# Kernel tuning notes

Hardware: AMD Instinct MI355X
Metric: run time of the kernel (lower is better)

## Reference

```python
import jax, jax.numpy as jnp
import numpy as np

V, D, H, B, LK, LQ, PAD = 10000, 300, 512, 16, 64, 64, 0


def _lstm(x, Wih, Whh, b, h0, c0):
    # x: [B,T,D]; Wih: [4G,D]; Whh: [4G,G]; b: [4G] (b_ih+b_hh); torch gate order i,f,g,o
    xg = jnp.einsum('btd,gd->btg', x, Wih) + b
    def step(hc, xt):
        h, c = hc
        g = xt + h @ Whh.T
        i, f, gg, o = jnp.split(g, 4, axis=-1)
        c = jax.nn.sigmoid(f) * c + jax.nn.sigmoid(i) * jnp.tanh(gg)
        h = jax.nn.sigmoid(o) * jnp.tanh(c)
        return (h, c), h
    (hT, cT), hs = jax.lax.scan(step, (h0, c0), jnp.swapaxes(xg, 0, 1))
    return jnp.swapaxes(hs, 0, 1), hT, cT


def setup_inputs() -> dict:
    key = jax.random.key(0)
    ks = jax.random.split(key, 24)
    n = lambda k, s: (jax.random.normal(k, s, jnp.float32) * 0.05)
    return {
        'source': jax.random.randint(ks[0], (B, LK), 0, V),
        'prev_outputs': jax.random.randint(ks[1], (B, LQ), 0, V),
        'emb': n(ks[2], (V, D)),
        'enc_f_Wih': n(ks[3], (4 * H, D)), 'enc_f_Whh': n(ks[4], (4 * H, H)), 'enc_f_b': n(ks[5], (4 * H,)),
        'enc_b_Wih': n(ks[6], (4 * H, D)), 'enc_b_Whh': n(ks[7], (4 * H, H)), 'enc_b_b': n(ks[8], (4 * H,)),
        'dec_Wih': n(ks[9], (8 * H, D)), 'dec_Whh': n(ks[10], (8 * H, 2 * H)), 'dec_b': n(ks[11], (8 * H,)),
        'k_W': n(ks[12], (2 * H, 2 * H)), 'k_b': n(ks[13], (2 * H,)),
        'v_W': n(ks[14], (2 * H, 2 * H)), 'v_b': n(ks[15], (2 * H,)),
        'fc1_W': n(ks[16], (2 * H, 4 * H)), 'fc1_b': n(ks[17], (2 * H,)),
        'fc2_W': n(ks[18], (V, 2 * H)), 'fc2_b': n(ks[19], (V,)),
    }


def reference(source, prev_outputs, emb, enc_f_Wih, enc_f_Whh, enc_f_b,
              enc_b_Wih, enc_b_Whh, enc_b_b, dec_Wih, dec_Whh, dec_b,
              k_W, k_b, v_W, v_b, fc1_W, fc1_b, fc2_W, fc2_b):
    bsz = source.shape[0]
    xs = emb[source]  # [B,LK,300]
    z = jnp.zeros((bsz, H), xs.dtype)
    out_f, hf, cf = _lstm(xs, enc_f_Wih, enc_f_Whh, enc_f_b, z, z)
    out_b, hb, cb = _lstm(xs[:, ::-1], enc_b_Wih, enc_b_Whh, enc_b_b, z, z)
    enc_out = jnp.concatenate([out_f, out_b[:, ::-1]], axis=-1)  # [B,LK,1024]
    # self.change: interleave fwd/bwd channels -> [B,1024]
    h0 = jnp.stack([hf, hb], axis=-1).reshape(bsz, 2 * H)
    c0 = jnp.stack([cf, cb], axis=-1).reshape(bsz, 2 * H)
    Q, _, _ = _lstm(emb[prev_outputs], dec_Wih, dec_Whh, dec_b, h0, c0)  # [B,LQ,1024]
    K = enc_out @ k_W.T + k_b
    Vv = enc_out @ v_W.T + v_b
    M = jnp.einsum('bqc,bkc->bqk', Q, K)
    mask = (source == PAD)[:, None, :]
    M = jnp.where(mask, -jnp.inf, M)
    A = jax.nn.softmax(M, axis=2)
    ctx = jnp.einsum('bqk,bkc->bqc', A, Vv)  # == (A[...,None]*V[:,None]).sum(2)
    x = jnp.tanh(jnp.concatenate([ctx, Q], axis=-1) @ fc1_W.T + fc1_b)  # dropout=identity (eval)
    return x @ fc2_W.T + fc2_b
```

## Files before the change

### kernel.cpp

```cpp
#include <hip/hip_runtime.h>
#include <cmath>

#define BB   16
#define LKK  64
#define LQQ  64
#define DD   300
#define HH   512
#define H2   1024
#define G4   2048
#define G8   4096
#define VV   10000

__device__ __forceinline__ float sigmoidf_(float x) { return 1.f / (1.f + expf(-x)); }

typedef __attribute__((ext_vector_type(4))) float    f4_;
typedef __attribute__((ext_vector_type(4))) unsigned u4_;

__device__ __forceinline__ void st_sc(float* p, float v) {
    __hip_atomic_store(p, v, __ATOMIC_RELAXED, __HIP_MEMORY_SCOPE_AGENT);
}

__device__ __forceinline__ f4_ ld4_sc(const float* p) {
    f4_ r;
    asm volatile("global_load_dwordx4 %0, %1, off sc0 sc1" : "=v"(r) : "v"(p));
    return r;
}
__device__ __forceinline__ u4_ ld4u_sc(const unsigned* p) {
    u4_ r;
    asm volatile("global_load_dwordx4 %0, %1, off sc0 sc1" : "=v"(r) : "v"(p));
    return r;
}
__device__ __forceinline__ void wait_vm0() {
    asm volatile("s_waitcnt vmcnt(0)" ::: "memory");
    __builtin_amdgcn_sched_barrier(0);
}

__device__ __forceinline__ void gbar2(unsigned* flags, int wg, unsigned target) {
    asm volatile("s_waitcnt vmcnt(0)" ::: "memory");
    if (threadIdx.x == 0)
        __hip_atomic_store(&flags[wg], target, __ATOMIC_RELAXED, __HIP_MEMORY_SCOPE_AGENT);
    if (threadIdx.x < 64) {
        for (;;) {
            u4_ f = ld4u_sc(flags + (threadIdx.x << 2));
            wait_vm0();
            unsigned m0 = f[0] < f[1] ? f[0] : f[1];
            unsigned m1 = f[2] < f[3] ? f[2] : f[3];
            unsigned mn = m0 < m1 ? m0 : m1;
            if (__all((int)(mn >= target))) break;
            __builtin_amdgcn_s_sleep(1);
        }
    }
    __syncthreads();
}

__global__ void rev_idx_kernel(const int* __restrict__ src, int* __restrict__ rev,
                               unsigned* __restrict__ bars) {
    int tid = blockIdx.x * blockDim.x + threadIdx.x;
    if (tid < 512) bars[tid] = 0u;
    if (tid < BB * LKK) {
        int b = tid / LKK, t = tid % LKK;
        rev[tid] = src[b * LKK + (LKK - 1 - t)];
    }
}

typedef __attribute__((ext_vector_type(8))) short bfrag8;
typedef __attribute__((ext_vector_type(4))) float facc4;

__device__ __forceinline__ unsigned short f2bf(float x) {
    unsigned u = __float_as_uint(x);
    unsigned r = (u + 0x7fffu + ((u >> 16) & 1u)) >> 16;
    return (unsigned short)r;
}

#define ASTR 40

__device__ __forceinline__ void gemm_core(
        short* __restrict__ Ah, short* __restrict__ Al,
        short* __restrict__ Bh, short* __restrict__ Bl,
        const float* __restrict__ A, const int* __restrict__ gidx, int lda,
        const float* __restrict__ Bw, int ldb,
        const float* __restrict__ bias,
        float* __restrict__ C, int ldc,
        int N, int K, int act, int m0, int n0) {
    int tid = threadIdx.x;
    int lane = tid & 63, w = tid >> 6;
    int wr = w >> 1, wc = w & 1;
    int fr = lane & 15, fg = lane >> 4;

    int sr = tid >> 1, sc = (tid & 1) << 4;
    long abase = gidx ? (long)gidx[m0 + sr] * lda : (long)(m0 + sr) * lda;
    int gn = n0 + sr;
    bool bval = gn < N;
    long bbase = (long)gn * ldb;

    facc4 acc[4][4] = {};

    for (int k0 = 0; k0 < K; k0 += 32) {
        {
            float v[16];
            if (k0 + sc + 16 <= K) {
                const float* ap = A + abase + k0 + sc;
                float4 t0 = *(const float4*)(ap + 0);
                float4 t1 = *(const float4*)(ap + 4);
                float4 t2 = *(const float4*)(ap + 8);
                float4 t3 = *(const float4*)(ap + 12);
                v[0]=t0.x; v[1]=t0.y; v[2]=t0.z;  v[3]=t0.w;
                v[4]=t1.x; v[5]=t1.y; v[6]=t1.z;  v[7]=t1.w;
                v[8]=t2.x; v[9]=t2.y; v[10]=t2.z; v[11]=t2.w;
                v[12]=t3.x; v[13]=t3.y; v[14]=t3.z; v[15]=t3.w;
            } else {
#pragma unroll
                for (int c = 0; c < 16; c++) {
                    int k = k0 + sc + c;
                    v[c] = (k < K) ? A[abase + k] : 0.f;
                }
            }
            bfrag8 h0, h1, l0, l1;
#pragma unroll
            for (int c = 0; c < 8; c++) {
                unsigned short hb = f2bf(v[c]);
                float hf = __uint_as_float(((unsigned)hb) << 16);
                h0[c] = (short)hb; l0[c] = (short)f2bf(v[c] - hf);
            }
#pragma unroll
            for (int c = 0; c < 8; c++) {
                unsigned short hb = f2bf(v[8 + c]);
                float hf = __uint_as_float(((unsigned)hb) << 16);
                h1[c] = (short)hb; l1[c] = (short)f2bf(v[8 + c] - hf);
            }
            *(bfrag8*)&Ah[sr * ASTR + sc]     = h0;
            *(bfrag8*)&Ah[sr * ASTR + sc + 8] = h1;
            *(bfrag8*)&Al[sr * ASTR + sc]     = l0;
            *(bfrag8*)&Al[sr * ASTR + sc + 8] = l1;
        }
        {
            float v[16];
            if (bval && (k0 + sc + 16 <= K)) {
                const float* bp = Bw + bbase + k0 + sc;
                float4 t0 = *(const float4*)(bp + 0);
                float4 t1 = *(const float4*)(bp + 4);
                float4 t2 = *(const float4*)(bp + 8);
                float4 t3 = *(const float4*)(bp + 12);
                v[0]=t0.x; v[1]=t0.y; v[2]=t0.z;  v[3]=t0.w;
                v[4]=t1.x; v[5]=t1.y; v[6]=t1.z;  v[7]=t1.w;
                v[8]=t2.x; v[9]=t2.y; v[10]=t2.z; v[11]=t2.w;
                v[12]=t3.x; v[13]=t3.y; v[14]=t3.z; v[15]=t3.w;
            } else {
#pragma unroll
                for (int c = 0; c < 16; c++) {
                    int k = k0 + sc + c;
                    v[c] = (bval && k < K) ? Bw[bbase + k] : 0.f;
                }
            }
            bfrag8 h0, h1, l0, l1;
#pragma unroll
            for (int c = 0; c < 8; c++) {
                unsigned short hb = f2bf(v[c]);
                float hf = __uint_as_float(((unsigned)hb) << 16);
                h0[c] = (short)hb; l0[c] = (short)f2bf(v[c] - hf);
            }
#pragma unroll
            for (int c = 0; c < 8; c++) {
                unsigned short hb = f2bf(v[8 + c]);
                float hf = __uint_as_float(((unsigned)hb) << 16);
                h1[c] = (short)hb; l1[c] = (short)f2bf(v[8 + c] - hf);
            }
            *(bfrag8*)&Bh[sr * ASTR + sc]     = h0;
            *(bfrag8*)&Bh[sr * ASTR + sc + 8] = h1;
            *(bfrag8*)&Bl[sr * ASTR + sc]     = l0;
            *(bfrag8*)&Bl[sr * ASTR + sc + 8] = l1;
        }
        __syncthreads();

        bfrag8 ah[4], al[4], bh[4], bl[4];
#pragma unroll
        for (int i = 0; i < 4; i++) {
            int ar = wr * 64 + i * 16 + fr;
            ah[i] = *(const bfrag8*)&Ah[ar * ASTR + fg * 8];
            al[i] = *(const bfrag8*)&Al[ar * ASTR + fg * 8];
            int br = wc * 64 + i * 16 + fr;
            bh[i] = *(const bfrag8*)&Bh[br * ASTR + fg * 8];
            bl[i] = *(const bfrag8*)&Bl[br * ASTR + fg * 8];
        }
#pragma unroll
        for (int i = 0; i < 4; i++)
#pragma unroll
            for (int j = 0; j < 4; j++) {
                acc[i][j] = __builtin_amdgcn_mfma_f32_16x16x32_bf16(ah[i], bh[j], acc[i][j], 0, 0, 0);
                acc[i][j] = __builtin_amdgcn_mfma_f32_16x16x32_bf16(ah[i], bl[j], acc[i][j], 0, 0, 0);
                acc[i][j] = __builtin_amdgcn_mfma_f32_16x16x32_bf16(al[i], bh[j], acc[i][j], 0, 0, 0);
            }
        __syncthreads();
    }

#pragma unroll
    for (int i = 0; i < 4; i++) {
        int row = m0 + wr * 64 + i * 16 + fg * 4;
#pragma unroll
        for (int j = 0; j < 4; j++) {
            int col = n0 + wc * 64 + j * 16 + fr;
            if (col < N) {
                float bz = bias[col];
#pragma unroll
                for (int q = 0; q < 4; q++) {
                    float vv = acc[i][j][q] + bz;
                    if (act == 1) vv = tanhf(vv);
                    C[(long)(row + q) * ldc + col] = vv;
                }
            }
        }
    }
}

__global__ __launch_bounds__(256)
void gemm_mfma128(const float* __restrict__ A, const int* __restrict__ gidx, int lda,
                  const float* __restrict__ Bw, int ldb,
                  const float* __restrict__ bias,
                  float* __restrict__ C, int ldc,
                  int N, int K, int act) {
    __shared__ __align__(16) short Ah[128 * ASTR];
    __shared__ __align__(16) short Al[128 * ASTR];
    __shared__ __align__(16) short Bh[128 * ASTR];
    __shared__ __align__(16) short Bl[128 * ASTR];
    gemm_core(Ah, Al, Bh, Bl, A, gidx, lda, Bw, ldb, bias, C, ldc, N, K, act,
              blockIdx.x * 128, blockIdx.y * 128);
}

__global__ __launch_bounds__(256)
void gemm_kv(const float* __restrict__ enc_out,
             const float* __restrict__ kW, const float* __restrict__ kb,
             const float* __restrict__ vW, const float* __restrict__ vb,
             float* __restrict__ Kbuf, float* __restrict__ Vbuf) {
    __shared__ __align__(16) short Ah[128 * ASTR];
    __shared__ __align__(16) short Al[128 * ASTR];
    __shared__ __align__(16) short Bh[128 * ASTR];
    __shared__ __align__(16) short Bl[128 * ASTR];
    int ny = blockIdx.y;
    if (ny < 8)
        gemm_core(Ah, Al, Bh, Bl, enc_out, nullptr, H2, kW, H2, kb, Kbuf, H2,
                  H2, H2, 0, blockIdx.x * 128, ny * 128);
    else
        gemm_core(Ah, Al, Bh, Bl, enc_out, nullptr, H2, vW, H2, vb, Vbuf, H2,
                  H2, H2, 0, blockIdx.x * 128, (ny - 8) * 128);
}

__global__ __launch_bounds__(256)
void gemm_xg(const float* __restrict__ emb,
             const int* __restrict__ src, const int* __restrict__ rev,
             const int* __restrict__ prev,
             const float* __restrict__ Wf, const float* __restrict__ bf,
             const float* __restrict__ Wb, const float* __restrict__ bb,
             const float* __restrict__ Wd, const float* __restrict__ bd,
             float* __restrict__ xf, float* __restrict__ xb,
             float* __restrict__ xd) {
    __shared__ __align__(16) short Ah[128 * ASTR];
    __shared__ __align__(16) short Al[128 * ASTR];
    __shared__ __align__(16) short Bh[128 * ASTR];
    __shared__ __align__(16) short Bl[128 * ASTR];
    int ny = blockIdx.y;
    if (ny < 16)
        gemm_core(Ah, Al, Bh, Bl, emb, src, DD, Wf, DD, bf, xf, G4,
                  G4, DD, 0, blockIdx.x * 128, ny * 128);
    else if (ny < 32)
        gemm_core(Ah, Al, Bh, Bl, emb, rev, DD, Wb, DD, bb, xb, G4,
                  G4, DD, 0, blockIdx.x * 128, (ny - 16) * 128);
    else
        gemm_core(Ah, Al, Bh, Bl, emb, prev, DD, Wd, DD, bd, xd, G8,
                  G8, DD, 0, blockIdx.x * 128, (ny - 32) * 128);
}

__global__ __launch_bounds__(256, 1)
void enc_recur(const float* __restrict__ xg_f, const float* __restrict__ xg_b,
               const float* __restrict__ Wf, const float* __restrict__ Wb,
               float* __restrict__ hglob, float* __restrict__ enc_out,
               float* __restrict__ encc, unsigned* __restrict__ flags) {
    __shared__ float hs[HH * 16];
    __shared__ float red[256 * 33];
    __shared__ float g256[256];
    __shared__ float hout[64];
    int wg  = blockIdx.x;
    int dir = wg >> 7;
    int j0  = (wg & 127) * 4;
    int tid = threadIdx.x;
    int ks   = tid & 31;
    int tile = tid >> 5;
    int bh   = tile >> 2;
    int gate = tile & 3;
    int sw   = (ks >> 2) & 3;
    const float* W  = dir ? Wb : Wf;
    const float* xg = dir ? xg_b : xg_f;

    float wreg[4][16];
#pragma unroll
    for (int jn = 0; jn < 4; jn++) {
        const float* wrow = W + (long)(gate * HH + j0 + jn) * HH;
#pragma unroll
        for (int j = 0; j < 16; j++) wreg[jn][j] = wrow[ks + 32 * j];
    }

    int ub = tid & 15, ujj = tid >> 4;
    int xb = tid >> 4, xgate = (tid >> 2) & 3, xjn = tid & 3;
    float creg = 0.f;
    float4* hsv = (float4*)hs;

    for (int t = 0; t < LKK; t++) {
        float acc[8][4];
#pragma unroll
        for (int i = 0; i < 8; i++)
#pragma unroll
            for (int jn = 0; jn < 4; jn++) acc[i][jn] = 0.f;

        auto do_fma = [&](int jlo, int jhi) {
#pragma unroll
            for (int j = jlo; j < jhi; j++) {
                int k = ks + 32 * j;
                float4 h0 = hsv[k * 4 + ((bh * 2 + 0) ^ sw)];
                float4 h1 = hsv[k * 4 + ((bh * 2 + 1) ^ sw)];
#pragma unroll
                for (int jn = 0; jn < 4; jn++) {
                    float w = wreg[jn][j];
                    acc[0][jn] += h0.x * w; acc[1][jn] += h0.y * w;
                    acc[2][jn] += h0.z * w; acc[3][jn] += h0.w * w;
                    acc[4][jn] += h1.x * w; acc[5][jn] += h1.y * w;
                    acc[6][jn] += h1.z * w; acc[7][jn] += h1.w * w;
                }
            }
        };

        float xval = xg[(long)(xb * LKK + t) * G4 + xgate * HH + j0 + xjn];

        if (t == 0) {
            for (int i = tid; i < HH * 16; i += 256) hs[i] = 0.f;
            __syncthreads();
            do_fma(0, 16);
        } else {
            const float* hg = hglob + (long)((dir << 1) | (t & 1)) * (HH * 16);
            f4_ vv[8];
#pragma unroll
            for (int u = 0; u < 8; u++) vv[u] = ld4_sc(hg + tid * 4 + u * 1024);
            asm volatile("s_waitcnt vmcnt(4)" ::: "memory");
            __builtin_amdgcn_sched_barrier(0);
#pragma unroll
            for (int u = 0; u < 4; u++) {
                int e = tid * 4 + u * 1024;
                int jj = e >> 4, b0 = e & 15;
                *(f4_*)&hs[(jj << 4) + ((((b0 >> 2) ^ ((jj >> 2) & 3))) << 2)] = vv[u];
            }
            __syncthreads();
            do_fma(0, 8);
            wait_vm0();
#pragma unroll
            for (int u = 4; u < 8; u++) {
                int e = tid * 4 + u * 1024;
                int jj = e >> 4, b0 = e & 15;
                *(f4_*)&hs[(jj << 4) + ((((b0 >> 2) ^ ((jj >> 2) & 3))) << 2)] = vv[u];
            }
            __syncthreads();
            do_fma(8, 16);
        }

#pragma unroll
        for (int i = 0; i < 8; i++)
#pragma unroll
            for (int jn = 0; jn < 4; jn++)
                red[((bh * 8 + i) * 16 + gate * 4 + jn) * 33 + ks] = acc[i][jn];
        __syncthreads();
        {
            const float* row = red + tid * 33;
            float s0 = 0.f, s1 = 0.f, s2 = 0.f, s3 = 0.f;
#pragma unroll
            for (int u = 0; u < 8; u++) {
                s0 += row[u * 4 + 0]; s1 += row[u * 4 + 1];
                s2 += row[u * 4 + 2]; s3 += row[u * 4 + 3];
            }
            g256[tid] = ((s0 + s1) + (s2 + s3)) + xval;
        }
        __syncthreads();

        if (tid < 64) {
            int j = j0 + ujj;
            float gi = g256[ub * 16 + 0  + ujj];
            float gf = g256[ub * 16 + 4  + ujj];
            float gg = g256[ub * 16 + 8  + ujj];
            float go = g256[ub * 16 + 12 + ujj];
            float cv = sigmoidf_(gf) * creg + sigmoidf_(gi) * tanhf(gg);
            creg = cv;
            float hv = sigmoidf_(go) * tanhf(cv);
            st_sc(&hglob[(long)((dir << 1) | ((t + 1) & 1)) * (HH * 16) + j * 16 + ub], hv);
            hout[tid] = hv;
            if (t == LKK - 1) encc[(dir * BB + ub) * HH + j] = creg;
        }
        if (t < LKK - 1) gbar2(flags, wg, (unsigned)(t + 1));
        else __syncthreads();
        if (tid >= 64 && tid < 128) {
            int lt = tid - 64;
            int j = j0 + (lt >> 4);
            int kpos = dir ? (LKK - 1 - t) : t;
            enc_out[(long)((lt & 15) * LKK + kpos) * H2 + dir * HH + j] = hout[lt];
        }
    }
}

__global__ __launch_bounds__(256, 1)
void dec_recur(const float* __restrict__ xg_d, const float* __restrict__ Wd,
               const float* __restrict__ enc_out, const float* __restrict__ encc,
               float* __restrict__ hglob, float* __restrict__ Qout,
               unsigned* __restrict__ flags) {
    __shared__ float hs[HH * 16];
    __shared__ float red[256 * 33];
    __shared__ float g256[256];
    __shared__ float hout[64];
    int wg  = blockIdx.x;
    int j0  = wg * 4;
    int tid = threadIdx.x;
    int ks   = tid & 31;
    int tile = tid >> 5;
    int bh   = tile >> 2;
    int gate = tile & 3;
    int sw   = (ks >> 2) & 3;

    float wreg[4][32];
#pragma unroll
    for (int jn = 0; jn < 4; jn++) {
        const float* wrow = Wd + (long)(gate * H2 + j0 + jn) * H2;
#pragma unroll
        for (int j = 0; j < 32; j++) wreg[jn][j] = wrow[ks + 32 * j];
    }

    int ub = tid & 15, ujj = tid >> 4;
    int xb = tid >> 4, xgate = (tid >> 2) & 3, xjn = tid & 3;
    float creg = 0.f;
    if (tid < 64) {
        int j = j0 + ujj;
        creg = ((j & 1) == 0) ? encc[ub * HH + (j >> 1)]
                              : encc[(BB + ub) * HH + (j >> 1)];
    }
    float4* hsv = (float4*)hs;

    for (int t = 0; t < LQQ; t++) {
        float xval = xg_d[(long)(xb * LQQ + t) * G8 + xgate * H2 + j0 + xjn];
        float acc[8][4];
#pragma unroll
        for (int i = 0; i < 8; i++)
#pragma unroll
            for (int jn = 0; jn < 4; jn++) acc[i][jn] = 0.f;

        auto do_fma = [&](int half) {
#pragma unroll
            for (int jj2 = 0; jj2 < 16; jj2++) {
                int j = half * 16 + jj2;
                int kl = ks + 32 * jj2;
                float4 h0 = hsv[kl * 4 + ((bh * 2 + 0) ^ sw)];
                float4 h1 = hsv[kl * 4 + ((bh * 2 + 1) ^ sw)];
#pragma unroll
                for (int jn = 0; jn < 4; jn++) {
                    float w = wreg[jn][j];
                    acc[0][jn] += h0.x * w; acc[1][jn] += h0.y * w;
                    acc[2][jn] += h0.z * w; acc[3][jn] += h0.w * w;
                    acc[4][jn] += h1.x * w; acc[5][jn] += h1.y * w;
                    acc[6][jn] += h1.z * w; acc[7][jn] += h1.w * w;
                }
            }
        };

        if (t == 0) {
            for (int half = 0; half < 2; half++) {
                for (int e = tid; e < HH * 16; e += 256) {
                    int kl = e >> 4, b = e & 15;
                    int k = half * HH + kl;
                    float hv = ((k & 1) == 0)
                        ? enc_out[(long)(b * LKK + (LKK - 1)) * H2 + (k >> 1)]
                        : enc_out[(long)(b * LKK) * H2 + HH + (k >> 1)];
                    hs[(kl << 4) + ((((b >> 2) ^ ((kl >> 2) & 3))) << 2) + (b & 3)] = hv;
                }
                __syncthreads();
                do_fma(half);
                __syncthreads();
            }
        } else {
            const float* hgA = hglob + (long)(t & 1) * (H2 * 16);
            f4_ vvA[8], vvB[8];
#pragma unroll
            for (int u = 0; u < 8; u++) vvA[u] = ld4_sc(hgA + tid * 4 + u * 1024);
#pragma unroll
            for (int u = 0; u < 8; u++) vvB[u] = ld4_sc(hgA + (HH * 16) + tid * 4 + u * 1024);
            asm volatile("s_waitcnt vmcnt(8)" ::: "memory");
            __builtin_amdgcn_sched_barrier(0);
#pragma unroll
            for (int u = 0; u < 8; u++) {
                int e = tid * 4 + u * 1024;
                int kl = e >> 4, b0 = e & 15;
                *(f4_*)&hs[(kl << 4) + ((((b0 >> 2) ^ ((kl >> 2) & 3))) << 2)] = vvA[u];
            }
            __syncthreads();
            do_fma(0);
            __syncthreads();
            wait_vm0();
#pragma unroll
            for (int u = 0; u < 8; u++) {
                int e = tid * 4 + u * 1024;
                int kl = e >> 4, b0 = e & 15;
                *(f4_*)&hs[(kl << 4) + ((((b0 >> 2) ^ ((kl >> 2) & 3))) << 2)] = vvB[u];
            }
            __syncthreads();
            do_fma(1);
        }

#pragma unroll
        for (int i = 0; i < 8; i++)
#pragma unroll
            for (int jn = 0; jn < 4; jn++)
                red[((bh * 8 + i) * 16 + gate * 4 + jn) * 33 + ks] = acc[i][jn];
        __syncthreads();
        {
            const float* row = red + tid * 33;
            float s0 = 0.f, s1 = 0.f, s2 = 0.f, s3 = 0.f;
#pragma unroll
            for (int u = 0; u < 8; u++) {
                s0 += row[u * 4 + 0]; s1 += row[u * 4 + 1];
                s2 += row[u * 4 + 2]; s3 += row[u * 4 + 3];
            }
            g256[tid] = ((s0 + s1) + (s2 + s3)) + xval;
        }
        __syncthreads();

        if (tid < 64) {
            int j = j0 + ujj;
            float gi = g256[ub * 16 + 0  + ujj];
            float gf = g256[ub * 16 + 4  + ujj];
            float gg = g256[ub * 16 + 8  + ujj];
            float go = g256[ub * 16 + 12 + ujj];
            float cv = sigmoidf_(gf) * creg + sigmoidf_(gi) * tanhf(gg);
            creg = cv;
            float hv = sigmoidf_(go) * tanhf(cv);
            st_sc(&hglob[(long)((t + 1) & 1) * (H2 * 16) + j * 16 + ub], hv);
            hout[tid] = hv;
        }
        if (t < LQQ - 1) gbar2(flags, wg, (unsigned)(t + 1));
        else __syncthreads();
        if (tid >= 64 && tid < 128) {
            int lt = tid - 64;
            int j = j0 + (lt >> 4);
            Qout[(long)((lt & 15) * LQQ + t) * H2 + j] = hout[lt];
        }
    }
}

__global__ __launch_bounds__(256)
void attention_kernel(const float* __restrict__ Qm, const float* __restrict__ Km,
                      const float* __restrict__ Vm, const int* __restrict__ source,
                      float* __restrict__ concatBuf) {
    int b = blockIdx.x >> 6;
    int q = blockIdx.x & 63;
    int tid = threadIdx.x;
    __shared__ float qrow[H2];
    __shared__ float part[LKK][4];
    __shared__ float aw[LKK];

    for (int i = tid; i < H2; i += 256) qrow[i] = Qm[(long)(b * LQQ + q) * H2 + i];
    __syncthreads();

    int k = tid >> 2, p = tid & 3;
    {
        const float* krow = Km + (long)(b * LKK + k) * H2 + p * 256;
        const float* qp = qrow + p * 256;
        float s = 0.f;
#pragma unroll 4
        for (int i = 0; i < 256; i++) s += qp[i] * krow[i];
        part[k][p] = s;
    }
    __syncthreads();
    if (tid < 64) {
        float sc = part[tid][0] + part[tid][1] + part[tid][2] + part[tid][3];
        bool masked = (source[b * LKK + tid] == 0);
        float m = masked ? -INFINITY : sc;
#pragma unroll
        for (int o = 32; o >= 1; o >>= 1) m = fmaxf(m, __shfl_xor(m, o, 64));
        float e = masked ? 0.f : expf(sc - m);
        float sum = e;
#pragma unroll
        for (int o = 32; o >= 1; o >>= 1) sum += __shfl_xor(sum, o, 64);
        aw[tid] = e / sum;
    }
    __syncthreads();

    for (int c = tid; c < H2; c += 256) {
        float acc = 0.f;
#pragma unroll 8
        for (int kk = 0; kk < LKK; kk++) acc += aw[kk] * Vm[(long)(b * LKK + kk) * H2 + c];
        long row = (long)(b * LQQ + q) * (2 * H2);
        concatBuf[row + c] = acc;
        concatBuf[row + H2 + c] = qrow[c];
    }
}

extern "C" void kernel_launch(void* const* d_in, const int* in_sizes, int n_in,
                              void* d_out, int out_size, void* d_ws, size_t ws_size,
                              hipStream_t stream) {
    const int*   src       = (const int*)  d_in[0];
    const int*   prev      = (const int*)  d_in[1];
    const float* emb       = (const float*)d_in[2];
    const float* enc_f_Wih = (const float*)d_in[3];
    const float* enc_f_Whh = (const float*)d_in[4];
    const float* enc_f_b   = (const float*)d_in[5];
    const float* enc_b_Wih = (const float*)d_in[6];
    const float* enc_b_Whh = (const float*)d_in[7];
    const float* enc_b_b   = (const float*)d_in[8];
    const float* dec_Wih   = (const float*)d_in[9];
    const float* dec_Whh   = (const float*)d_in[10];
    const float* dec_b     = (const float*)d_in[11];
    const float* k_W  = (const float*)d_in[12];
    const float* k_b  = (const float*)d_in[13];
    const float* v_W  = (const float*)d_in[14];
    const float* v_b  = (const float*)d_in[15];
    const float* fc1_W = (const float*)d_in[16];
    const float* fc1_b = (const float*)d_in[17];
    const float* fc2_W = (const float*)d_in[18];
    const float* fc2_b = (const float*)d_in[19];
    float* out = (float*)d_out;

    float* p = (float*)d_ws;
    float* xg_f    = p; p += (long)BB * LKK * G4;
    float* xg_b    = p; p += (long)BB * LKK * G4;
    float* xg_d    = p; p += (long)BB * LQQ * G8;
    float* enc_out = p; p += (long)BB * LKK * H2;
    float* encc    = p; p += 2L * BB * HH;
    float* hg_enc  = p; p += 2L * 2 * HH * 16;
    float* hg_dec  = p; p += 2L * H2 * 16;
    float* Qbuf    = p; p += (long)BB * LQQ * H2;
    float* Kbuf    = p; p += (long)BB * LKK * H2;
    float* Vbuf    = p; p += (long)BB * LKK * H2;
    float* concatB = p; p += (long)BB * LQQ * 2 * H2;
    float* fc1out  = p; p += (long)BB * LQQ * H2;
    int*   rev     = (int*)p; p += (BB * LKK);
    unsigned* bars = (unsigned*)p; p += 512;

    rev_idx_kernel<<<4, 256, 0, stream>>>(src, rev, bars);

    gemm_xg<<<dim3(8, 64), 256, 0, stream>>>(emb, src, rev, prev,
                                             enc_f_Wih, enc_f_b,
                                             enc_b_Wih, enc_b_b,
                                             dec_Wih, dec_b,
                                             xg_f, xg_b, xg_d);

    enc_recur<<<dim3(256), dim3(256), 0, stream>>>(xg_f, xg_b, enc_f_Whh, enc_b_Whh,
                                                   hg_enc, enc_out, encc, bars);

    gemm_kv<<<dim3(8, 16), 256, 0, stream>>>(enc_out, k_W, k_b, v_W, v_b, Kbuf, Vbuf);

    dec_recur<<<dim3(256), dim3(256), 0, stream>>>(xg_d, dec_Whh, enc_out, encc,
                                                   hg_dec, Qbuf, bars + 256);

    attention_kernel<<<BB * LQQ, 256, 0, stream>>>(Qbuf, Kbuf, Vbuf, src, concatB);

    gemm_mfma128<<<dim3(8, 8), 256, 0, stream>>>(concatB, nullptr, 2 * H2, fc1_W, 2 * H2,
                                                 fc1_b, fc1out, H2, H2, 2 * H2, 1);

    gemm_mfma128<<<dim3(8, (VV + 127) / 128), 256, 0, stream>>>(fc1out, nullptr, H2, fc2_W, H2,
                                                                fc2_b, out, VV, VV, H2, 0);
}
```

Baseline: 1.592 ms.

## Split encoder grid barrier per direction and pipeline flag polling loads

The encoder's grid-wide barrier now synchronises only the 128 workgroups of the same LSTM direction, using a separate flag array per direction, so the forward and backward recurrences no longer wait on each other. The polling loop in both barriers keeps one flag load in flight while checking the previous one, and the sleep between polls is removed. This aims to cut barrier latency on the serial recurrence critical path, at the cost of more aggressive memory polling traffic.

```diff
diff --git a/kernel.cpp b/kernel.cpp
--- a/kernel.cpp
+++ b/kernel.cpp
@@ -15,6 +15,7 @@
 
 typedef __attribute__((ext_vector_type(4))) float    f4_;
 typedef __attribute__((ext_vector_type(4))) unsigned u4_;
+typedef __attribute__((ext_vector_type(2))) unsigned u2_;
 
 __device__ __forceinline__ void st_sc(float* p, float v) {
     __hip_atomic_store(p, v, __ATOMIC_RELAXED, __HIP_MEMORY_SCOPE_AGENT);
@@ -30,25 +31,64 @@
     asm volatile("global_load_dwordx4 %0, %1, off sc0 sc1" : "=v"(r) : "v"(p));
     return r;
 }
+__device__ __forceinline__ u2_ ld2u_sc(const unsigned* p) {
+    u2_ r;
+    asm volatile("global_load_dwordx2 %0, %1, off sc0 sc1" : "=v"(r) : "v"(p));
+    return r;
+}
 __device__ __forceinline__ void wait_vm0() {
     asm volatile("s_waitcnt vmcnt(0)" ::: "memory");
     __builtin_amdgcn_sched_barrier(0);
 }
-
-__device__ __forceinline__ void gbar2(unsigned* flags, int wg, unsigned target) {
+__device__ __forceinline__ void wait_vm1() {
+    asm volatile("s_waitcnt vmcnt(1)" ::: "memory");
+    __builtin_amdgcn_sched_barrier(0);
+}
+
+__device__ __forceinline__ void gbar256(unsigned* flags, int wg, unsigned target) {
     asm volatile("s_waitcnt vmcnt(0)" ::: "memory");
     if (threadIdx.x == 0)
         __hip_atomic_store(&flags[wg], target, __ATOMIC_RELAXED, __HIP_MEMORY_SCOPE_AGENT);
     if (threadIdx.x < 64) {
+        const unsigned* p = flags + (threadIdx.x << 2);
+        u4_ f0 = ld4u_sc(p);
         for (;;) {
-            u4_ f = ld4u_sc(flags + (threadIdx.x << 2));
-            wait_vm0();
-            unsigned m0 = f[0] < f[1] ? f[0] : f[1];
-            unsigned m1 = f[2] < f[3] ? f[2] : f[3];
-            unsigned mn = m0 < m1 ? m0 : m1;
+            u4_ f1 = ld4u_sc(p);
+            wait_vm1();
+            unsigned m0 = f0[0] < f0[1] ? f0[0] : f0[1];
+            unsigned m1 = f0[2] < f0[3] ? f0[2] : f0[3];
+            if (__all((int)((m0 < m1 ? m0 : m1) >= target))) break;
+            u4_ f2 = ld4u_sc(p);
+            wait_vm1();
+            m0 = f1[0] < f1[1] ? f1[0] : f1[1];
+            m1 = f1[2] < f1[3] ? f1[2] : f1[3];
+            if (__all((int)((m0 < m1 ? m0 : m1) >= target))) break;
+            f0 = f2;
+        }
+        wait_vm0();
+    }
+    __syncthreads();
+}
+
+__device__ __forceinline__ void gbar128(unsigned* flags, int wg, unsigned target) {
+    asm volatile("s_waitcnt vmcnt(0)" ::: "memory");
+    if (threadIdx.x == 0)
+        __hip_atomic_store(&flags[wg], target, __ATOMIC_RELAXED, __HIP_MEMORY_SCOPE_AGENT);
+    if (threadIdx.x < 64) {
+        const unsigned* p = flags + (threadIdx.x << 1);
+        u2_ f0 = ld2u_sc(p);
+        for (;;) {
+            u2_ f1 = ld2u_sc(p);
+            wait_vm1();
+            unsigned mn = f0[0] < f0[1] ? f0[0] : f0[1];
             if (__all((int)(mn >= target))) break;
-            __builtin_amdgcn_s_sleep(1);
-        }
+            u2_ f2 = ld2u_sc(p);
+            wait_vm1();
+            mn = f1[0] < f1[1] ? f1[0] : f1[1];
+            if (__all((int)(mn >= target))) break;
+            f0 = f2;
+        }
+        wait_vm0();
     }
     __syncthreads();
 }
@@ -289,6 +329,8 @@
     int sw   = (ks >> 2) & 3;
     const float* W  = dir ? Wb : Wf;
     const float* xg = dir ? xg_b : xg_f;
+    unsigned* fl = flags + (dir << 7);
+    int wgl = wg & 127;
 
     float wreg[4][16];
 #pragma unroll
@@ -390,7 +432,7 @@
             hout[tid] = hv;
             if (t == LKK - 1) encc[(dir * BB + ub) * HH + j] = creg;
         }
-        if (t < LKK - 1) gbar2(flags, wg, (unsigned)(t + 1));
+        if (t < LKK - 1) gbar128(fl, wgl, (unsigned)(t + 1));
         else __syncthreads();
         if (tid >= 64 && tid < 128) {
             int lt = tid - 64;
@@ -536,7 +578,7 @@
             st_sc(&hglob[(long)((t + 1) & 1) * (H2 * 16) + j * 16 + ub], hv);
             hout[tid] = hv;
         }
-        if (t < LQQ - 1) gbar2(flags, wg, (unsigned)(t + 1));
+        if (t < LQQ - 1) gbar256(flags, wg, (unsigned)(t + 1));
         else __syncthreads();
         if (tid >= 64 && tid < 128) {
             int lt = tid - 64;
```

Result: faster. 1.528 ms (-4.0%).
